# Kernel optimization log

Hardware: AMD Instinct MI355X
Metric: run time of the kernel (lower is better)

## Reference

```python
import jax, jax.numpy as jnp
import numpy as np

N = 50000
E = 800000
F_IN = 128
H = 8        # heads
C = 32       # hidden_channels per head
HC = H * C   # 256
NEG_SLOPE = 0.2


def setup_inputs() -> dict:
    key = jax.random.key(0)
    ks = jax.random.split(key, 16)
    s = 0.1
    return {
        'x': jax.random.normal(ks[0], (N, F_IN), jnp.float32),
        'edge_index': jax.random.randint(ks[1], (2, E), 0, N, jnp.int64),
        'edge_weights': jax.random.uniform(ks[2], (E,), jnp.float32),
        'W1': jax.random.normal(ks[3], (F_IN, HC), jnp.float32) * s,
        'att_src1': jax.random.normal(ks[4], (H, C), jnp.float32) * s,
        'att_dst1': jax.random.normal(ks[5], (H, C), jnp.float32) * s,
        'b1': jnp.zeros((HC,), jnp.float32),
        'W2': jax.random.normal(ks[6], (HC, HC), jnp.float32) * s,
        'att_src2': jax.random.normal(ks[7], (H, C), jnp.float32) * s,
        'att_dst2': jax.random.normal(ks[8], (H, C), jnp.float32) * s,
        'b2': jnp.zeros((HC,), jnp.float32),
        'We': jax.random.normal(ks[9], (HC, 1), jnp.float32) * s,
        'be': jnp.zeros((1,), jnp.float32),
        'Wn': jax.random.normal(ks[10], (HC, 1), jnp.float32) * s,
        'bn': jnp.zeros((1,), jnp.float32),
    }


def gat_conv(x, src, dst, W, att_src, att_dst, bias):
    """PyG GATConv (concat=True, eval mode, self-loops already in src/dst)."""
    n = x.shape[0]
    h = (x @ W).reshape(n, H, C)                      # [N,H,C]
    a_s = jnp.sum(h * att_src, axis=-1)               # [N,H]
    a_d = jnp.sum(h * att_dst, axis=-1)               # [N,H]
    e = jax.nn.leaky_relu(a_s[src] + a_d[dst], NEG_SLOPE)  # [E',H]
    m = jax.ops.segment_max(e, dst, num_segments=n)   # segment softmax over dst
    ex = jnp.exp(e - m[dst])
    denom = jax.ops.segment_sum(ex, dst, num_segments=n)
    alpha = ex / (denom[dst] + 1e-16)                 # [E',H]
    out = jax.ops.segment_sum(alpha[..., None] * h[src], dst, num_segments=n)
    return out.reshape(n, HC) + bias


def reference(x, edge_index, edge_weights, W1, att_src1, att_dst1, b1,
              W2, att_src2, att_dst2, b2, We, be, Wn, bn):
    src0, dst0 = edge_index[0], edge_index[1]
    loops = jnp.arange(N, dtype=src0.dtype)
    src = jnp.concatenate([src0, loops])
    dst = jnp.concatenate([dst0, loops])
    # edge_weights is passed to GATConv as edge_attr but unused (edge_dim=None)
    h = jax.nn.relu(gat_conv(x, src, dst, W1, att_src1, att_dst1, b1))
    h = jax.nn.relu(gat_conv(h, src, dst, W2, att_src2, att_dst2, b2))
    edge_pred = (h[src0] * h[dst0]) @ We + be          # [E,1]
    node_pred = h @ Wn + bn                            # [N,1]
    return (edge_pred, node_pred)
```

## Files before the change

### kernel.cpp

```cpp
#include <hip/hip_runtime.h>
#include <hip/hip_bf16.h>

#define NN 50000
#define NE 800000
#define FIN 128
#define HC 256
#define NEG_SLOPE 0.2f

#define GEMM_BLOCKS 1564
#define NSB 3321
#define NB_ZERO 196
#define NB_X 6250
#define NB_W1 128
#define NB_W2 256

typedef short bf16x8 __attribute__((ext_vector_type(8)));
typedef float f32x4 __attribute__((ext_vector_type(4)));

__device__ __forceinline__ unsigned short f2bf(float f) {
  unsigned u = __float_as_uint(f);
  u += 0x7fff + ((u >> 16) & 1);
  return (unsigned short)(u >> 16);
}
__device__ __forceinline__ float bf2f(unsigned short s) {
  return __uint_as_float((unsigned)s << 16);
}
__device__ __forceinline__ float bflo(unsigned u) { return __uint_as_float(u << 16); }
__device__ __forceinline__ float bfhi(unsigned u) { return __uint_as_float(u & 0xffff0000u); }

__global__ __launch_bounds__(256) void prep_kernel(
    const float* __restrict__ X, unsigned short* __restrict__ Xh,
    const float* __restrict__ W1, unsigned short* __restrict__ W1th,
    unsigned short* __restrict__ W1tl, const float* __restrict__ W2,
    unsigned short* __restrict__ W2th, unsigned short* __restrict__ W2tl,
    int* __restrict__ counts, int* __restrict__ tmp) {
  int b = blockIdx.x, t = threadIdx.x;
  if (b < NB_ZERO) {
    int i = b * 256 + t;
    if (i < NN) { counts[i] = 0; tmp[i] = 0; }
  } else if (b < NB_ZERO + NB_X) {
    int i = (b - NB_ZERO) * 256 + t;
    float4 v = ((const float4*)X)[i];
    ushort4 h;
    h.x = f2bf(v.x); h.y = f2bf(v.y); h.z = f2bf(v.z); h.w = f2bf(v.w);
    ((ushort4*)Xh)[i] = h;
  } else if (b < NB_ZERO + NB_X + NB_W1) {
    int j = (b - NB_ZERO - NB_X) * 256 + t;
    int n = j >> 7, k = j & 127;
    float v = W1[k * HC + n];
    unsigned short h = f2bf(v);
    W1th[j] = h;
    W1tl[j] = f2bf(v - bf2f(h));
  } else {
    int j = (b - NB_ZERO - NB_X - NB_W1) * 256 + t;
    int n = j >> 8, k = j & 255;
    float v = W2[k * HC + n];
    unsigned short h = f2bf(v);
    W2th[j] = h;
    W2tl[j] = f2bf(v - bf2f(h));
  }
}

__global__ __launch_bounds__(256) void gemm_coef(
    const unsigned short* __restrict__ A, const unsigned short* __restrict__ Bth,
    const unsigned short* __restrict__ Btl, const float* __restrict__ att_s,
    const float* __restrict__ att_d, unsigned short* __restrict__ Cb,
    float* __restrict__ a_s, float* __restrict__ a_d, int M, int K,
    const int* __restrict__ ei, const int* __restrict__ rowptr,
    int* __restrict__ tmpc, int2* __restrict__ ce) {
  __shared__ unsigned short sA[64 * 40];
  __shared__ unsigned short sBh[128 * 40];
  __shared__ unsigned short sBl[128 * 40];
  __shared__ float sCS[64][4];
  __shared__ float sCD[64][4];

  int bid = blockIdx.x, t = threadIdx.x;
  if (bid >= GEMM_BLOCKS) {
    int e = (bid - GEMM_BLOCKS) * 256 + t;
    if (e < NE + NN) {
      int s, d, id;
      if (e < NE) { s = ei[e]; d = ei[NE + e]; id = e; }
      else { s = d = e - NE; id = -1; }
      int pos = rowptr[d] + atomicAdd(&tmpc[d], 1);
      ce[pos] = make_int2(s, id);
    }
    return;
  }

  int w = t >> 6, lane = t & 63;
  int quad = lane >> 4, lrow = lane & 15;
  int m0 = (bid >> 1) * 64, n0 = (bid & 1) * 128;
  int rm = (w & 1) * 32, cn = (w >> 1) * 64;

  f32x4 acc[2][4] = {};

  for (int k0 = 0; k0 < K; k0 += 32) {
    {
      int row = t >> 2, q = t & 3;
      int gm = m0 + row;
      if (gm >= M) gm = M - 1;
      *(uint4*)(sA + row * 40 + q * 8) = *(const uint4*)(A + (size_t)gm * K + k0 + q * 8);
    }
#pragma unroll
    for (int i = 0; i < 2; ++i) {
      int idx = t + i * 256;
      int row = idx >> 2, q = idx & 3;
      size_t gb = (size_t)(n0 + row) * K + k0 + q * 8;
      *(uint4*)(sBh + row * 40 + q * 8) = *(const uint4*)(Bth + gb);
      *(uint4*)(sBl + row * 40 + q * 8) = *(const uint4*)(Btl + gb);
    }
    __syncthreads();

    bf16x8 fa[2];
#pragma unroll
    for (int mi = 0; mi < 2; ++mi)
      fa[mi] = *(const bf16x8*)(sA + (rm + mi * 16 + lrow) * 40 + quad * 8);
#pragma unroll
    for (int ni = 0; ni < 4; ++ni) {
      bf16x8 fbh = *(const bf16x8*)(sBh + (cn + ni * 16 + lrow) * 40 + quad * 8);
      bf16x8 fbl = *(const bf16x8*)(sBl + (cn + ni * 16 + lrow) * 40 + quad * 8);
#pragma unroll
      for (int mi = 0; mi < 2; ++mi) {
        acc[mi][ni] = __builtin_amdgcn_mfma_f32_16x16x32_bf16(fa[mi], fbh, acc[mi][ni], 0, 0, 0);
        acc[mi][ni] = __builtin_amdgcn_mfma_f32_16x16x32_bf16(fa[mi], fbl, acc[mi][ni], 0, 0, 0);
      }
    }
    __syncthreads();
  }

  float vs[4], vd[4];
#pragma unroll
  for (int ni = 0; ni < 4; ++ni) {
    int gn = n0 + cn + ni * 16 + lrow;
    vs[ni] = att_s[gn];
    vd[ni] = att_d[gn];
  }
  int h4e = cn >> 5;

#pragma unroll
  for (int mi = 0; mi < 2; ++mi) {
#pragma unroll
    for (int r = 0; r < 4; ++r) {
      int lr = rm + mi * 16 + quad * 4 + r;
      int gm = m0 + lr;
      if (gm < M) {
#pragma unroll
        for (int ni = 0; ni < 4; ++ni) {
          int gn = n0 + cn + ni * 16 + lrow;
          Cb[(size_t)gm * HC + gn] = f2bf(acc[mi][ni][r]);
        }
      }
      float pse = acc[mi][0][r] * vs[0] + acc[mi][1][r] * vs[1];
      float pso = acc[mi][2][r] * vs[2] + acc[mi][3][r] * vs[3];
      float pde = acc[mi][0][r] * vd[0] + acc[mi][1][r] * vd[1];
      float pdo = acc[mi][2][r] * vd[2] + acc[mi][3][r] * vd[3];
#pragma unroll
      for (int off = 1; off <= 8; off <<= 1) {
        pse += __shfl_xor(pse, off);
        pso += __shfl_xor(pso, off);
        pde += __shfl_xor(pde, off);
        pdo += __shfl_xor(pdo, off);
      }
      if (lrow == 0) {
        sCS[lr][h4e] = pse;
        sCS[lr][h4e + 1] = pso;
        sCD[lr][h4e] = pde;
        sCD[lr][h4e + 1] = pdo;
      }
    }
  }
  __syncthreads();
  if (t < 64) {
    int gm = m0 + t;
    if (gm < M) {
      int o = (n0 >> 5);
      *(float4*)(a_s + (size_t)gm * 8 + o) = *(const float4*)&sCS[t][0];
      *(float4*)(a_d + (size_t)gm * 8 + o) = *(const float4*)&sCD[t][0];
    }
  }
}

__global__ void hist_kernel(const int* __restrict__ ei, int* __restrict__ counts) {
  int e = blockIdx.x * 256 + threadIdx.x;
  if (e < NE) atomicAdd(&counts[ei[NE + e]], 1);
}

__global__ void scan1(const int* __restrict__ counts, int* __restrict__ scanbuf,
                      int* __restrict__ bsum) {
  __shared__ int sd[256];
  int t = threadIdx.x;
  int i = blockIdx.x * 256 + t;
  int v = (i < NN) ? counts[i] + 1 : 0;
  sd[t] = v;
  __syncthreads();
#pragma unroll
  for (int off = 1; off < 256; off <<= 1) {
    int x = (t >= off) ? sd[t - off] : 0;
    __syncthreads();
    sd[t] += x;
    __syncthreads();
  }
  if (i < NN) scanbuf[i] = sd[t];
  if (t == 255) bsum[blockIdx.x] = sd[255];
}

__global__ void scan2(const int* __restrict__ bsum, int* __restrict__ boff, int nb) {
  __shared__ int sd[256];
  int t = threadIdx.x;
  int v = (t < nb) ? bsum[t] : 0;
  sd[t] = v;
  __syncthreads();
#pragma unroll
  for (int off = 1; off < 256; off <<= 1) {
    int x = (t >= off) ? sd[t - off] : 0;
    __syncthreads();
    sd[t] += x;
    __syncthreads();
  }
  if (t < nb) boff[t] = sd[t] - v;
}

__global__ void scan3(const int* __restrict__ scanbuf, const int* __restrict__ boff,
                      int* __restrict__ rowptr) {
  int i = blockIdx.x * 256 + threadIdx.x;
  if (i < NN) rowptr[i + 1] = scanbuf[i] + boff[blockIdx.x];
  if (i == 0) rowptr[0] = 0;
}

__global__ __launch_bounds__(256) void agg_kernel(
    const unsigned short* __restrict__ htb, const float* __restrict__ a_s,
    const float* __restrict__ a_d, const int* __restrict__ rowptr,
    const int2* __restrict__ ce, const float* __restrict__ bias,
    unsigned short* __restrict__ outb,
    const float* __restrict__ Wn, const float* __restrict__ bn,
    float* __restrict__ outn) {
  int d = blockIdx.x * 8 + (threadIdx.x >> 5);
  if (d >= NN) return;
  int l = threadIdx.x & 31;
  int hh = l >> 2;
  float adh = a_d[d * 8 + hh];
  int r0 = rowptr[d], r1 = rowptr[d + 1];
  float denom = 0.f;
  float4 acc0 = {0.f, 0.f, 0.f, 0.f};
  float4 acc1 = {0.f, 0.f, 0.f, 0.f};
  for (int r = r0; r < r1; r += 4) {
    int s[4];
    float as_[4];
    uint4 q[4];
    bool ok[4];
#pragma unroll
    for (int j = 0; j < 4; ++j) {
      int rj = r + j;
      ok[j] = rj < r1;
      rj = ok[j] ? rj : r1 - 1;
      s[j] = ce[rj].x;
    }
#pragma unroll
    for (int j = 0; j < 4; ++j) {
      as_[j] = a_s[s[j] * 8 + hh];
      q[j] = ((const uint4*)(htb + (size_t)s[j] * HC))[l];
    }
#pragma unroll
    for (int j = 0; j < 4; ++j) {
      float e = as_[j] + adh;
      e = e > 0.f ? e : NEG_SLOPE * e;
      float w = ok[j] ? __expf(e) : 0.f;
      denom += w;
      acc0.x += w * bflo(q[j].x);
      acc0.y += w * bfhi(q[j].x);
      acc0.z += w * bflo(q[j].y);
      acc0.w += w * bfhi(q[j].y);
      acc1.x += w * bflo(q[j].z);
      acc1.y += w * bfhi(q[j].z);
      acc1.z += w * bflo(q[j].w);
      acc1.w += w * bfhi(q[j].w);
    }
  }
  float dv = 1.f / denom;
  float4 b0 = *(const float4*)(bias + l * 8);
  float4 b1 = *(const float4*)(bias + l * 8 + 4);
  float4 o0, o1;
  o0.x = fmaxf(fmaf(acc0.x, dv, b0.x), 0.f);
  o0.y = fmaxf(fmaf(acc0.y, dv, b0.y), 0.f);
  o0.z = fmaxf(fmaf(acc0.z, dv, b0.z), 0.f);
  o0.w = fmaxf(fmaf(acc0.w, dv, b0.w), 0.f);
  o1.x = fmaxf(fmaf(acc1.x, dv, b1.x), 0.f);
  o1.y = fmaxf(fmaf(acc1.y, dv, b1.y), 0.f);
  o1.z = fmaxf(fmaf(acc1.z, dv, b1.z), 0.f);
  o1.w = fmaxf(fmaf(acc1.w, dv, b1.w), 0.f);
  uint4 pb;
  pb.x = (unsigned)f2bf(o0.x) | ((unsigned)f2bf(o0.y) << 16);
  pb.y = (unsigned)f2bf(o0.z) | ((unsigned)f2bf(o0.w) << 16);
  pb.z = (unsigned)f2bf(o1.x) | ((unsigned)f2bf(o1.y) << 16);
  pb.w = (unsigned)f2bf(o1.z) | ((unsigned)f2bf(o1.w) << 16);
  ((uint4*)(outb + (size_t)d * HC))[l] = pb;
  if (outn) {
    const float4* wnp = (const float4*)(Wn + l * 8);
    float4 w0 = wnp[0], w1 = wnp[1];
    float p = o0.x * w0.x + o0.y * w0.y + o0.z * w0.z + o0.w * w0.w +
              o1.x * w1.x + o1.y * w1.y + o1.z * w1.z + o1.w * w1.w;
#pragma unroll
    for (int off = 1; off <= 16; off <<= 1) p += __shfl_xor(p, off);
    if (l == 0) outn[d] = p + bn[0];
  }
}

__global__ __launch_bounds__(256) void edge_pred_kernel(
    const unsigned short* __restrict__ h2b, const int* __restrict__ rowptr,
    const int2* __restrict__ ce, const float* __restrict__ We,
    const float* __restrict__ be, float* __restrict__ out) {
  int d = blockIdx.x * 4 + (threadIdx.x >> 6);
  if (d >= NN) return;
  int lane = threadIdx.x & 63;
  int g = lane >> 4, l = lane & 15;
  float b = be[0];

  const uint4* rowd = (const uint4*)(h2b + (size_t)d * HC + l * 16);
  uint4 qd0 = rowd[0], qd1 = rowd[1];
  float wd[16];
  {
    const float4* wep = (const float4*)(We + l * 16);
    float4 w0 = wep[0], w1 = wep[1], w2 = wep[2], w3 = wep[3];
    wd[0] = bflo(qd0.x) * w0.x;  wd[1] = bfhi(qd0.x) * w0.y;
    wd[2] = bflo(qd0.y) * w0.z;  wd[3] = bfhi(qd0.y) * w0.w;
    wd[4] = bflo(qd0.z) * w1.x;  wd[5] = bfhi(qd0.z) * w1.y;
    wd[6] = bflo(qd0.w) * w1.z;  wd[7] = bfhi(qd0.w) * w1.w;
    wd[8] = bflo(qd1.x) * w2.x;  wd[9] = bfhi(qd1.x) * w2.y;
    wd[10] = bflo(qd1.y) * w2.z; wd[11] = bfhi(qd1.y) * w2.w;
    wd[12] = bflo(qd1.z) * w3.x; wd[13] = bfhi(qd1.z) * w3.y;
    wd[14] = bflo(qd1.w) * w3.z; wd[15] = bfhi(qd1.w) * w3.w;
  }

  int r0 = rowptr[d], r1 = rowptr[d + 1];
  for (int r = r0; r < r1; r += 8) {
    int rr0 = r + g, rr1 = r + 4 + g;
    int s0 = 0, id0 = -1, s1 = 0, id1 = -1;
    if (rr0 < r1) { int2 p = ce[rr0]; s0 = p.x; id0 = p.y; }
    if (rr1 < r1) { int2 p = ce[rr1]; s1 = p.x; id1 = p.y; }
    const uint4* ra = (const uint4*)(h2b + (size_t)s0 * HC + l * 16);
    const uint4* rb = (const uint4*)(h2b + (size_t)s1 * HC + l * 16);
    uint4 a0 = ra[0], a1 = ra[1];
    uint4 c0 = rb[0], c1 = rb[1];
    float p0 = bflo(a0.x) * wd[0] + bfhi(a0.x) * wd[1] + bflo(a0.y) * wd[2] +
               bfhi(a0.y) * wd[3] + bflo(a0.z) * wd[4] + bfhi(a0.z) * wd[5] +
               bflo(a0.w) * wd[6] + bfhi(a0.w) * wd[7] + bflo(a1.x) * wd[8] +
               bfhi(a1.x) * wd[9] + bflo(a1.y) * wd[10] + bfhi(a1.y) * wd[11] +
               bflo(a1.z) * wd[12] + bfhi(a1.z) * wd[13] + bflo(a1.w) * wd[14] +
               bfhi(a1.w) * wd[15];
    float p1 = bflo(c0.x) * wd[0] + bfhi(c0.x) * wd[1] + bflo(c0.y) * wd[2] +
               bfhi(c0.y) * wd[3] + bflo(c0.z) * wd[4] + bfhi(c0.z) * wd[5] +
               bflo(c0.w) * wd[6] + bfhi(c0.w) * wd[7] + bflo(c1.x) * wd[8] +
               bfhi(c1.x) * wd[9] + bflo(c1.y) * wd[10] + bfhi(c1.y) * wd[11] +
               bflo(c1.z) * wd[12] + bfhi(c1.z) * wd[13] + bflo(c1.w) * wd[14] +
               bfhi(c1.w) * wd[15];
#pragma unroll
    for (int off = 1; off <= 8; off <<= 1) {
      p0 += __shfl_xor(p0, off);
      p1 += __shfl_xor(p1, off);
    }
    if (l == 0) {
      if (id0 >= 0) out[id0] = p0 + b;
      if (id1 >= 0) out[id1] = p1 + b;
    }
  }
}

extern "C" void kernel_launch(void* const* d_in, const int* in_sizes, int n_in,
                              void* d_out, int out_size, void* d_ws, size_t ws_size,
                              hipStream_t stream) {
  const float* x  = (const float*)d_in[0];
  const int* ei   = (const int*)d_in[1];
  const float* W1 = (const float*)d_in[3];
  const float* as1 = (const float*)d_in[4];
  const float* ad1 = (const float*)d_in[5];
  const float* b1 = (const float*)d_in[6];
  const float* W2 = (const float*)d_in[7];
  const float* as2 = (const float*)d_in[8];
  const float* ad2 = (const float*)d_in[9];
  const float* b2 = (const float*)d_in[10];
  const float* We = (const float*)d_in[11];
  const float* be = (const float*)d_in[12];
  const float* Wn = (const float*)d_in[13];
  const float* bn = (const float*)d_in[14];
  float* out = (float*)d_out;

  char* wsp = (char*)d_ws;
  auto alloc = [&](size_t bytes) {
    char* p = wsp;
    wsp += (bytes + 255) & ~(size_t)255;
    return p;
  };
  unsigned short* hbA = (unsigned short*)alloc((size_t)NN * HC * 2);
  unsigned short* h1b = (unsigned short*)alloc((size_t)NN * HC * 2);
  unsigned short* hbB = (unsigned short*)alloc((size_t)NN * HC * 2);
  float* a_s = (float*)alloc((size_t)NN * 8 * 4);
  float* a_d = (float*)alloc((size_t)NN * 8 * 4);
  int* rowptr = (int*)alloc((size_t)(NN + 1) * 4);
  int2* ce = (int2*)alloc((size_t)(NE + NN + 8) * 8);
  int* counts = (int*)alloc((size_t)NN * 4);
  int* tmp = (int*)alloc((size_t)NN * 4);
  int* scanbuf = (int*)alloc((size_t)NN * 4);
  int* bsum = (int*)alloc(256 * 4);
  int* boff = (int*)alloc(256 * 4);
  unsigned short* W1th = (unsigned short*)alloc((size_t)FIN * HC * 2);
  unsigned short* W1tl = (unsigned short*)alloc((size_t)FIN * HC * 2);
  unsigned short* W2th = (unsigned short*)alloc((size_t)HC * HC * 2);
  unsigned short* W2tl = (unsigned short*)alloc((size_t)HC * HC * 2);

  unsigned short* xh = h1b;

  const int NB = (NN + 255) / 256;

  prep_kernel<<<NB_ZERO + NB_X + NB_W1 + NB_W2, 256, 0, stream>>>(
      x, xh, W1, W1th, W1tl, W2, W2th, W2tl, counts, tmp);
  hist_kernel<<<(NE + 255) / 256, 256, 0, stream>>>(ei, counts);
  scan1<<<NB, 256, 0, stream>>>(counts, scanbuf, bsum);
  scan2<<<1, 256, 0, stream>>>(bsum, boff, NB);
  scan3<<<NB, 256, 0, stream>>>(scanbuf, boff, rowptr);

  gemm_coef<<<GEMM_BLOCKS + NSB, 256, 0, stream>>>(
      xh, W1th, W1tl, as1, ad1, hbA, a_s, a_d, NN, FIN, ei, rowptr, tmp, ce);
  agg_kernel<<<NN / 8, 256, 0, stream>>>(hbA, a_s, a_d, rowptr, ce, b1, h1b,
                                         (const float*)nullptr, (const float*)nullptr,
                                         (float*)nullptr);

  gemm_coef<<<GEMM_BLOCKS, 256, 0, stream>>>(
      h1b, W2th, W2tl, as2, ad2, hbA, a_s, a_d, NN, HC,
      (const int*)nullptr, rowptr, tmp, ce);
  agg_kernel<<<NN / 8, 256, 0, stream>>>(hbA, a_s, a_d, rowptr, ce, b2, hbB,
                                         Wn, bn, out + NE);

  edge_pred_kernel<<<NN / 4, 256, 0, stream>>>(hbB, rowptr, ce, We, be, out);
}
```

Measured before the change: 437.4 us.

## Fuse histogram into prep, partition CSR scatter by destination, widen aggregation to wavefront

Result: no change. 439.0 us (+0.4%).

```diff
diff --git a/kernel.cpp b/kernel.cpp
--- a/kernel.cpp
+++ b/kernel.cpp
@@ -8,8 +8,8 @@
 #define NEG_SLOPE 0.2f
 
 #define GEMM_BLOCKS 1564
-#define NSB 3321
-#define NB_ZERO 196
+#define NSCAT 3328
+#define NB_HIST 782
 #define NB_X 6250
 #define NB_W1 128
 #define NB_W2 256
@@ -28,31 +28,34 @@
 __device__ __forceinline__ float bflo(unsigned u) { return __uint_as_float(u << 16); }
 __device__ __forceinline__ float bfhi(unsigned u) { return __uint_as_float(u & 0xffff0000u); }
 
-__global__ __launch_bounds__(256) void prep_kernel(
+__global__ __launch_bounds__(256) void prep_hist(
     const float* __restrict__ X, unsigned short* __restrict__ Xh,
     const float* __restrict__ W1, unsigned short* __restrict__ W1th,
     unsigned short* __restrict__ W1tl, const float* __restrict__ W2,
     unsigned short* __restrict__ W2th, unsigned short* __restrict__ W2tl,
-    int* __restrict__ counts, int* __restrict__ tmp) {
+    const int* __restrict__ ei, int* __restrict__ counts) {
   int b = blockIdx.x, t = threadIdx.x;
-  if (b < NB_ZERO) {
-    int i = b * 256 + t;
-    if (i < NN) { counts[i] = 0; tmp[i] = 0; }
-  } else if (b < NB_ZERO + NB_X) {
-    int i = (b - NB_ZERO) * 256 + t;
+  if (b < NB_HIST) {
+#pragma unroll
+    for (int u = 0; u < 4; ++u) {
+      int e = b * 1024 + u * 256 + t;
+      if (e < NE) atomicAdd(&counts[ei[NE + e]], 1);
+    }
+  } else if (b < NB_HIST + NB_X) {
+    int i = (b - NB_HIST) * 256 + t;
     float4 v = ((const float4*)X)[i];
     ushort4 h;
     h.x = f2bf(v.x); h.y = f2bf(v.y); h.z = f2bf(v.z); h.w = f2bf(v.w);
     ((ushort4*)Xh)[i] = h;
-  } else if (b < NB_ZERO + NB_X + NB_W1) {
-    int j = (b - NB_ZERO - NB_X) * 256 + t;
+  } else if (b < NB_HIST + NB_X + NB_W1) {
+    int j = (b - NB_HIST - NB_X) * 256 + t;
     int n = j >> 7, k = j & 127;
     float v = W1[k * HC + n];
     unsigned short h = f2bf(v);
     W1th[j] = h;
     W1tl[j] = f2bf(v - bf2f(h));
   } else {
-    int j = (b - NB_ZERO - NB_X - NB_W1) * 256 + t;
+    int j = (b - NB_HIST - NB_X - NB_W1) * 256 + t;
     int n = j >> 8, k = j & 255;
     float v = W2[k * HC + n];
     unsigned short h = f2bf(v);
@@ -67,7 +70,7 @@
     const float* __restrict__ att_d, unsigned short* __restrict__ Cb,
     float* __restrict__ a_s, float* __restrict__ a_d, int M, int K,
     const int* __restrict__ ei, const int* __restrict__ rowptr,
-    int* __restrict__ tmpc, int2* __restrict__ ce) {
+    int* __restrict__ tmpc, int2* __restrict__ ce, int scat) {
   __shared__ unsigned short sA[64 * 40];
   __shared__ unsigned short sBh[128 * 40];
   __shared__ unsigned short sBl[128 * 40];
@@ -75,21 +78,29 @@
   __shared__ float sCD[64][4];
 
   int bid = blockIdx.x, t = threadIdx.x;
-  if (bid >= GEMM_BLOCKS) {
-    int e = (bid - GEMM_BLOCKS) * 256 + t;
-    if (e < NE + NN) {
-      int s, d, id;
-      if (e < NE) { s = ei[e]; d = ei[NE + e]; id = e; }
-      else { s = d = e - NE; id = -1; }
-      int pos = rowptr[d] + atomicAdd(&tmpc[d], 1);
-      ce[pos] = make_int2(s, id);
+  if (bid < scat) {
+    int x = bid & 7;
+    int c = bid >> 3;
+#pragma unroll
+    for (int u = 0; u < 8; ++u) {
+      int e = c * 2048 + u * 256 + t;
+      if (e < NE + NN) {
+        int d = (e < NE) ? ei[NE + e] : e - NE;
+        if ((unsigned)d / 6250u == (unsigned)x) {
+          int s  = (e < NE) ? ei[e] : d;
+          int id = (e < NE) ? e : -1;
+          int pos = rowptr[d] + atomicAdd(&tmpc[d], 1);
+          ce[pos] = make_int2(s, id);
+        }
+      }
     }
     return;
   }
 
+  int gb = bid - scat;
   int w = t >> 6, lane = t & 63;
   int quad = lane >> 4, lrow = lane & 15;
-  int m0 = (bid >> 1) * 64, n0 = (bid & 1) * 128;
+  int m0 = (gb >> 1) * 64, n0 = (gb & 1) * 128;
   int rm = (w & 1) * 32, cn = (w >> 1) * 64;
 
   f32x4 acc[2][4] = {};
@@ -105,9 +116,9 @@
     for (int i = 0; i < 2; ++i) {
       int idx = t + i * 256;
       int row = idx >> 2, q = idx & 3;
-      size_t gb = (size_t)(n0 + row) * K + k0 + q * 8;
-      *(uint4*)(sBh + row * 40 + q * 8) = *(const uint4*)(Bth + gb);
-      *(uint4*)(sBl + row * 40 + q * 8) = *(const uint4*)(Btl + gb);
+      size_t gbx = (size_t)(n0 + row) * K + k0 + q * 8;
+      *(uint4*)(sBh + row * 40 + q * 8) = *(const uint4*)(Bth + gbx);
+      *(uint4*)(sBl + row * 40 + q * 8) = *(const uint4*)(Btl + gbx);
     }
     __syncthreads();
 
@@ -180,11 +191,6 @@
   }
 }
 
-__global__ void hist_kernel(const int* __restrict__ ei, int* __restrict__ counts) {
-  int e = blockIdx.x * 256 + threadIdx.x;
-  if (e < NE) atomicAdd(&counts[ei[NE + e]], 1);
-}
-
 __global__ void scan1(const int* __restrict__ counts, int* __restrict__ scanbuf,
                       int* __restrict__ bsum) {
   __shared__ int sd[256];
@@ -234,19 +240,18 @@
     unsigned short* __restrict__ outb,
     const float* __restrict__ Wn, const float* __restrict__ bn,
     float* __restrict__ outn) {
-  int d = blockIdx.x * 8 + (threadIdx.x >> 5);
+  int d = blockIdx.x * 4 + (threadIdx.x >> 6);
   if (d >= NN) return;
-  int l = threadIdx.x & 31;
-  int hh = l >> 2;
+  int l = threadIdx.x & 63;
+  int hh = l >> 3;
   float adh = a_d[d * 8 + hh];
   int r0 = rowptr[d], r1 = rowptr[d + 1];
   float denom = 0.f;
-  float4 acc0 = {0.f, 0.f, 0.f, 0.f};
-  float4 acc1 = {0.f, 0.f, 0.f, 0.f};
+  float4 acc = {0.f, 0.f, 0.f, 0.f};
   for (int r = r0; r < r1; r += 4) {
     int s[4];
     float as_[4];
-    uint4 q[4];
+    uint2 q[4];
     bool ok[4];
 #pragma unroll
     for (int j = 0; j < 4; ++j) {
@@ -258,7 +263,7 @@
 #pragma unroll
     for (int j = 0; j < 4; ++j) {
       as_[j] = a_s[s[j] * 8 + hh];
-      q[j] = ((const uint4*)(htb + (size_t)s[j] * HC))[l];
+      q[j] = ((const uint2*)(htb + (size_t)s[j] * HC))[l];
     }
 #pragma unroll
     for (int j = 0; j < 4; ++j) {
@@ -266,41 +271,28 @@
       e = e > 0.f ? e : NEG_SLOPE * e;
       float w = ok[j] ? __expf(e) : 0.f;
       denom += w;
-      acc0.x += w * bflo(q[j].x);
-      acc0.y += w * bfhi(q[j].x);
-      acc0.z += w * bflo(q[j].y);
-      acc0.w += w * bfhi(q[j].y);
-      acc1.x += w * bflo(q[j].z);
-      acc1.y += w * bfhi(q[j].z);
-      acc1.z += w * bflo(q[j].w);
-      acc1.w += w * bfhi(q[j].w);
+      acc.x += w * bflo(q[j].x);
+      acc.y += w * bfhi(q[j].x);
+      acc.z += w * bflo(q[j].y);
+      acc.w += w * bfhi(q[j].y);
     }
   }
   float dv = 1.f / denom;
-  float4 b0 = *(const float4*)(bias + l * 8);
-  float4 b1 = *(const float4*)(bias + l * 8 + 4);
-  float4 o0, o1;
-  o0.x = fmaxf(fmaf(acc0.x, dv, b0.x), 0.f);
-  o0.y = fmaxf(fmaf(acc0.y, dv, b0.y), 0.f);
-  o0.z = fmaxf(fmaf(acc0.z, dv, b0.z), 0.f);
-  o0.w = fmaxf(fmaf(acc0.w, dv, b0.w), 0.f);
-  o1.x = fmaxf(fmaf(acc1.x, dv, b1.x), 0.f);
-  o1.y = fmaxf(fmaf(acc1.y, dv, b1.y), 0.f);
-  o1.z = fmaxf(fmaf(acc1.z, dv, b1.z), 0.f);
-  o1.w = fmaxf(fmaf(acc1.w, dv, b1.w), 0.f);
-  uint4 pb;
-  pb.x = (unsigned)f2bf(o0.x) | ((unsigned)f2bf(o0.y) << 16);
-  pb.y = (unsigned)f2bf(o0.z) | ((unsigned)f2bf(o0.w) << 16);
-  pb.z = (unsigned)f2bf(o1.x) | ((unsigned)f2bf(o1.y) << 16);
-  pb.w = (unsigned)f2bf(o1.z) | ((unsigned)f2bf(o1.w) << 16);
-  ((uint4*)(outb + (size_t)d * HC))[l] = pb;
+  float4 bi = *(const float4*)(bias + l * 4);
+  float4 o;
+  o.x = fmaxf(fmaf(acc.x, dv, bi.x), 0.f);
+  o.y = fmaxf(fmaf(acc.y, dv, bi.y), 0.f);
+  o.z = fmaxf(fmaf(acc.z, dv, bi.z), 0.f);
+  o.w = fmaxf(fmaf(acc.w, dv, bi.w), 0.f);
+  uint2 pb;
+  pb.x = (unsigned)f2bf(o.x) | ((unsigned)f2bf(o.y) << 16);
+  pb.y = (unsigned)f2bf(o.z) | ((unsigned)f2bf(o.w) << 16);
+  ((uint2*)(outb + (size_t)d * HC))[l] = pb;
   if (outn) {
-    const float4* wnp = (const float4*)(Wn + l * 8);
-    float4 w0 = wnp[0], w1 = wnp[1];
-    float p = o0.x * w0.x + o0.y * w0.y + o0.z * w0.z + o0.w * w0.w +
-              o1.x * w1.x + o1.y * w1.y + o1.z * w1.z + o1.w * w1.w;
-#pragma unroll
-    for (int off = 1; off <= 16; off <<= 1) p += __shfl_xor(p, off);
+    float4 wv = *(const float4*)(Wn + l * 4);
+    float p = o.x * wv.x + o.y * wv.y + o.z * wv.z + o.w * wv.w;
+#pragma unroll
+    for (int off = 1; off <= 32; off <<= 1) p += __shfl_xor(p, off);
     if (l == 0) outn[d] = p + bn[0];
   }
 }
@@ -411,23 +403,25 @@
 
   const int NB = (NN + 255) / 256;
 
-  prep_kernel<<<NB_ZERO + NB_X + NB_W1 + NB_W2, 256, 0, stream>>>(
-      x, xh, W1, W1th, W1tl, W2, W2th, W2tl, counts, tmp);
-  hist_kernel<<<(NE + 255) / 256, 256, 0, stream>>>(ei, counts);
+  hipMemsetAsync(counts, 0, (size_t)NN * 4, stream);
+  hipMemsetAsync(tmp, 0, (size_t)NN * 4, stream);
+
+  prep_hist<<<NB_HIST + NB_X + NB_W1 + NB_W2, 256, 0, stream>>>(
+      x, xh, W1, W1th, W1tl, W2, W2th, W2tl, ei, counts);
   scan1<<<NB, 256, 0, stream>>>(counts, scanbuf, bsum);
   scan2<<<1, 256, 0, stream>>>(bsum, boff, NB);
   scan3<<<NB, 256, 0, stream>>>(scanbuf, boff, rowptr);
 
-  gemm_coef<<<GEMM_BLOCKS + NSB, 256, 0, stream>>>(
-      xh, W1th, W1tl, as1, ad1, hbA, a_s, a_d, NN, FIN, ei, rowptr, tmp, ce);
-  agg_kernel<<<NN / 8, 256, 0, stream>>>(hbA, a_s, a_d, rowptr, ce, b1, h1b,
+  gemm_coef<<<NSCAT + GEMM_BLOCKS, 256, 0, stream>>>(
+      xh, W1th, W1tl, as1, ad1, hbA, a_s, a_d, NN, FIN, ei, rowptr, tmp, ce, NSCAT);
+  agg_kernel<<<NN / 4, 256, 0, stream>>>(hbA, a_s, a_d, rowptr, ce, b1, h1b,
                                          (const float*)nullptr, (const float*)nullptr,
                                          (float*)nullptr);
 
   gemm_coef<<<GEMM_BLOCKS, 256, 0, stream>>>(
       h1b, W2th, W2tl, as2, ad2, hbA, a_s, a_d, NN, HC,
-      (const int*)nullptr, rowptr, tmp, ce);
-  agg_kernel<<<NN / 8, 256, 0, stream>>>(hbA, a_s, a_d, rowptr, ce, b2, hbB,
+      (const int*)nullptr, rowptr, tmp, ce, 0);
+  agg_kernel<<<NN / 4, 256, 0, stream>>>(hbA, a_s, a_d, rowptr, ce, b2, hbB,
                                          Wn, bn, out + NE);
 
   edge_pred_kernel<<<NN / 4, 256, 0, stream>>>(hbB, rowptr, ce, We, be, out);
```
